# Kernel tuning notes

Hardware: AMD Instinct MI355X
Metric: run time of the kernel (lower is better)

Reference implementation:

```python
import jax, jax.numpy as jnp
import numpy as np

EPS = 1e-12  # tf.math.l2_normalize epsilon

def _l2norm(x):
    # normalize over last axis, matching K.l2_normalize semantics
    sq = jnp.sum(x * x, axis=-1, keepdims=True)
    return x * jax.lax.rsqrt(jnp.maximum(sq, EPS))

def setup_inputs() -> dict:
    key = jax.random.key(0)
    k1, k2, k3 = jax.random.split(key, 3)
    B, L, D, P = 16, 256, 256, 20
    sent1 = jax.random.normal(k1, (B, L, D), dtype=jnp.float32)
    sent2 = jax.random.normal(k2, (B, L, D), dtype=jnp.float32)
    # glorot_uniform for shape (P, D)
    limit = np.sqrt(6.0 / (P + D)).astype(np.float32)
    kernel = jax.random.uniform(k3, (P, D), minval=-limit, maxval=limit, dtype=jnp.float32)
    return {"sent1": sent1, "sent2": sent2, "kernel": kernel}

def reference(sent1, sent2, kernel):
    # sent1: [B,L1,D], sent2: [B,L2,D], kernel: [P,D]
    v1 = _l2norm(sent1[:, :, None, :] * kernel)  # [B,L1,P,D]
    v2 = _l2norm(sent2[:, :, None, :] * kernel)  # [B,L2,P,D]
    # per-perspective cosine similarity matrix: [B,L1,L2,P]
    cos = jnp.einsum('blpd,bmpd->blmp', v1, v2)
    # max over the other sentence's positions (L2) -> [B,L1,P]
    return jnp.max(cos, axis=2)
```

## Files before the change

kernel.cpp:

```cpp
#include <hip/hip_runtime.h>
#include <hip/hip_bf16.h>


#define B_DIM 16
#define L_DIM 256
#define D_DIM 256
#define P_DIM 20
#define TL 64
#define TM 64
#define LDX 264
#define EPS 1e-12f

typedef __attribute__((ext_vector_type(8))) __bf16 bf16x8;
typedef __attribute__((ext_vector_type(4))) float f32x4;

__device__ __forceinline__ unsigned short f2bf(float x) {
  unsigned int u = __float_as_uint(x);
  u += 0x7fffu + ((u >> 16) & 1u);
  return (unsigned short)(u >> 16);
}

__global__ __launch_bounds__(256)
void prep_kernel(const float* __restrict__ s1, const float* __restrict__ s2,
                 const float* __restrict__ kg, float* __restrict__ rn1,
                 float* __restrict__ rn2, unsigned short* __restrict__ s2bf) {
  const int lane = threadIdx.x & 63;
  const int gw   = blockIdx.x * 4 + (threadIdx.x >> 6);
  const int sent = gw >> 12;
  const int row  = gw & 4095;
  const float* src = sent ? s2 : s1;
  float4 sv = *(const float4*)(src + (size_t)row * D_DIM + lane * 4);
  if (sent) {
    unsigned int p0 = ((unsigned int)f2bf(sv.y) << 16) | f2bf(sv.x);
    unsigned int p1 = ((unsigned int)f2bf(sv.w) << 16) | f2bf(sv.z);
    *(uint2*)&s2bf[(size_t)row * D_DIM + lane * 4] = make_uint2(p0, p1);
  }
  float q0 = sv.x * sv.x, q1 = sv.y * sv.y, q2 = sv.z * sv.z, q3 = sv.w * sv.w;
  float* rn = sent ? rn2 : rn1;
  const int b = row >> 8, l = row & 255;
  #pragma unroll 4
  for (int p = 0; p < P_DIM; ++p) {
    float4 kv = *(const float4*)(kg + p * D_DIM + lane * 4);
    float v = q0 * kv.x * kv.x + q1 * kv.y * kv.y + q2 * kv.z * kv.z + q3 * kv.w * kv.w;
    #pragma unroll
    for (int off = 1; off < 64; off <<= 1) v += __shfl_xor(v, off);
    if (lane == 0) rn[((size_t)b * P_DIM + p) * L_DIM + l] = rsqrtf(fmaxf(v, EPS));
  }
}

__global__ __launch_bounds__(256, 2)
void mpm_main(const float* __restrict__ s1, const unsigned short* __restrict__ s2bf,
              const float* __restrict__ kg, const float* __restrict__ rn1,
              const float* __restrict__ rn2, float* __restrict__ outg) {
  __shared__ __align__(16) unsigned short X1[TL * LDX];
  __shared__ __align__(16) unsigned short X2[TM * 256];
  __shared__ float RN1[TL];
  __shared__ float RN2[L_DIM];
  __shared__ float outtmp[2][TL];

  const int tid  = threadIdx.x;
  const int lane = tid & 63;
  const int wave = tid >> 6;
  const int wl = wave & 1, wm = wave >> 1;
  const int lr = lane & 15, q = lane >> 4;

  const int bid = blockIdx.x;
  const int lt = bid & 3;
  const int p  = (bid >> 2) % P_DIM;
  const int b  = bid / (4 * P_DIM);
  const int l0 = lt * TL;

  if (tid < TL) RN1[tid] = rn1[((size_t)b * P_DIM + p) * L_DIM + l0 + tid];
  RN2[tid] = rn2[((size_t)b * P_DIM + p) * L_DIM + tid];
  __syncthreads();

  float4 kv = *(const float4*)(kg + p * D_DIM + lane * 4);
  const float k0 = kv.x * kv.x, k1 = kv.y * kv.y, k2 = kv.z * kv.z, k3 = kv.w * kv.w;

  const float* s1b = s1 + ((size_t)b * L_DIM + l0) * D_DIM;
  #pragma unroll
  for (int i = 0; i < 16; ++i) {
    const int row = i * 4 + wave;
    float4 sv = *(const float4*)(s1b + row * D_DIM + lane * 4);
    float r = RN1[row];
    float x0 = sv.x * k0 * r, x1 = sv.y * k1 * r, x2 = sv.z * k2 * r, x3 = sv.w * k3 * r;
    unsigned int p0 = ((unsigned int)f2bf(x1) << 16) | f2bf(x0);
    unsigned int p1 = ((unsigned int)f2bf(x3) << 16) | f2bf(x2);
    *(uint2*)&X1[row * LDX + lane * 4] = make_uint2(p0, p1);
  }

  float rmax0 = -1e30f, rmax1 = -1e30f;
  const unsigned short* s2b = s2bf + (size_t)b * L_DIM * D_DIM;

  const int baseA0 = (wm * 32 + lr) * 256;
  const int baseA1 = baseA0 + 16 * 256;
  const unsigned short* b0p = &X1[(wl * 32 + lr) * LDX + q * 8];
  const unsigned short* b1p = &X1[(wl * 32 + 16 + lr) * LDX + q * 8];

  for (int mt = 0; mt < L_DIM / TM; ++mt) {
    if (mt) __syncthreads();
    {
      const unsigned short* srcb = s2b + mt * TM * 256;
      unsigned short* ldsb = &X2[wave * 64 * 8];
      #pragma unroll
      for (int j = 0; j < 8; ++j) {
        int sg = j * 256 + tid;
        int r  = sg >> 5, x = sg & 31;
        int c  = x ^ (r & 31);
        const unsigned short* g = srcb + r * 256 + c * 8;
        __builtin_amdgcn_global_load_lds(
            (const __attribute__((address_space(1))) void*)g,
            (__attribute__((address_space(3))) void*)(ldsb + j * 256 * 8),
            16, 0, 0);
      }
    }
    __syncthreads();

    f32x4 acc00 = {0,0,0,0}, acc01 = {0,0,0,0}, acc10 = {0,0,0,0}, acc11 = {0,0,0,0};
    #pragma unroll
    for (int kt = 0; kt < 8; ++kt) {
      const int cc = q + kt * 4;
      bf16x8 a0 = *(const bf16x8*)&X2[baseA0 + ((cc ^ lr) << 3)];
      bf16x8 a1 = *(const bf16x8*)&X2[baseA1 + ((cc ^ lr ^ 16) << 3)];
      bf16x8 b0 = *(const bf16x8*)(b0p + kt * 32);
      bf16x8 b1 = *(const bf16x8*)(b1p + kt * 32);
      acc00 = __builtin_amdgcn_mfma_f32_16x16x32_bf16(a0, b0, acc00, 0, 0, 0);
      acc01 = __builtin_amdgcn_mfma_f32_16x16x32_bf16(a0, b1, acc01, 0, 0, 0);
      acc10 = __builtin_amdgcn_mfma_f32_16x16x32_bf16(a1, b0, acc10, 0, 0, 0);
      acc11 = __builtin_amdgcn_mfma_f32_16x16x32_bf16(a1, b1, acc11, 0, 0, 0);
    }

    #pragma unroll
    for (int r = 0; r < 4; ++r) {
      float rm0 = RN2[mt * TM + wm * 32 + q * 4 + r];
      float rm1 = RN2[mt * TM + wm * 32 + 16 + q * 4 + r];
      rmax0 = fmaxf(rmax0, fmaxf(acc00[r] * rm0, acc10[r] * rm1));
      rmax1 = fmaxf(rmax1, fmaxf(acc01[r] * rm0, acc11[r] * rm1));
    }
  }

  rmax0 = fmaxf(rmax0, __shfl_xor(rmax0, 16));
  rmax0 = fmaxf(rmax0, __shfl_xor(rmax0, 32));
  rmax1 = fmaxf(rmax1, __shfl_xor(rmax1, 16));
  rmax1 = fmaxf(rmax1, __shfl_xor(rmax1, 32));
  if (q == 0) {
    outtmp[wm][wl * 32 + lr]      = rmax0;
    outtmp[wm][wl * 32 + 16 + lr] = rmax1;
  }
  __syncthreads();
  if (tid < TL)
    outg[((size_t)b * L_DIM + (l0 + tid)) * P_DIM + p] =
        fmaxf(outtmp[0][tid], outtmp[1][tid]);
}

extern "C" void kernel_launch(void* const* d_in, const int* in_sizes, int n_in,
                              void* d_out, int out_size, void* d_ws, size_t ws_size,
                              hipStream_t stream) {
  const float* s1 = (const float*)d_in[0];
  const float* s2 = (const float*)d_in[1];
  const float* kg = (const float*)d_in[2];
  float* out = (float*)d_out;

  float* rn1 = (float*)d_ws;
  float* rn2 = rn1 + (size_t)B_DIM * P_DIM * L_DIM;
  unsigned short* s2bf = (unsigned short*)(rn2 + (size_t)B_DIM * P_DIM * L_DIM);

  prep_kernel<<<dim3(2048), dim3(256), 0, stream>>>(s1, s2, kg, rn1, rn2, s2bf);
  mpm_main<<<dim3(B_DIM * P_DIM * (L_DIM / TL)), dim3(256), 0, stream>>>(
      s1, s2bf, kg, rn1, rn2, out);
}
```

Measured before the change: 96.99 us.

## Stage full s2 batch in LDS and loop perspectives per block

Each block now loads the entire bf16 s2 batch into LDS once and keeps its s1 rows in registers, iterating over five perspectives. Each wave computes a 64x64 output tile with 16 accumulators. This removes repeated global/L2 reloads of s2 and s1 across perspectives and m-tiles. In exchange it uses 160KB LDS with one block per CU, has only 256 blocks, and leaves no overlap of the initial load with compute.

```diff
diff --git a/kernel.cpp b/kernel.cpp
--- a/kernel.cpp
+++ b/kernel.cpp
@@ -6,9 +6,6 @@
 #define L_DIM 256
 #define D_DIM 256
 #define P_DIM 20
-#define TL 64
-#define TM 64
-#define LDX 264
 #define EPS 1e-12f
 
 typedef __attribute__((ext_vector_type(8))) __bf16 bf16x8;
@@ -48,109 +45,138 @@
   }
 }
 
-__global__ __launch_bounds__(256, 2)
+__global__ __launch_bounds__(256, 1)
 void mpm_main(const float* __restrict__ s1, const unsigned short* __restrict__ s2bf,
               const float* __restrict__ kg, const float* __restrict__ rn1,
               const float* __restrict__ rn2, float* __restrict__ outg) {
-  __shared__ __align__(16) unsigned short X1[TL * LDX];
-  __shared__ __align__(16) unsigned short X2[TM * 256];
-  __shared__ float RN1[TL];
-  __shared__ float RN2[L_DIM];
-  __shared__ float outtmp[2][TL];
+  __shared__ __align__(16) unsigned short X2[256 * 256];
+  __shared__ __align__(16) unsigned short X1[64 * 256];
+  float* WoutF = (float*)X1;
 
   const int tid  = threadIdx.x;
   const int lane = tid & 63;
   const int wave = tid >> 6;
-  const int wl = wave & 1, wm = wave >> 1;
-  const int lr = lane & 15, q = lane >> 4;
+  const int lr   = lane & 15;
+  const int q    = lane >> 4;
 
   const int bid = blockIdx.x;
-  const int lt = bid & 3;
-  const int p  = (bid >> 2) % P_DIM;
-  const int b  = bid / (4 * P_DIM);
-  const int l0 = lt * TL;
+  const int pgi = bid & 3;
+  const int lt  = (bid >> 2) & 3;
+  const int b   = bid >> 4;
+  const int l0  = lt * 64;
 
-  if (tid < TL) RN1[tid] = rn1[((size_t)b * P_DIM + p) * L_DIM + l0 + tid];
-  RN2[tid] = rn2[((size_t)b * P_DIM + p) * L_DIM + tid];
-  __syncthreads();
-
-  float4 kv = *(const float4*)(kg + p * D_DIM + lane * 4);
-  const float k0 = kv.x * kv.x, k1 = kv.y * kv.y, k2 = kv.z * kv.z, k3 = kv.w * kv.w;
-
-  const float* s1b = s1 + ((size_t)b * L_DIM + l0) * D_DIM;
-  #pragma unroll
-  for (int i = 0; i < 16; ++i) {
-    const int row = i * 4 + wave;
-    float4 sv = *(const float4*)(s1b + row * D_DIM + lane * 4);
-    float r = RN1[row];
-    float x0 = sv.x * k0 * r, x1 = sv.y * k1 * r, x2 = sv.z * k2 * r, x3 = sv.w * k3 * r;
-    unsigned int p0 = ((unsigned int)f2bf(x1) << 16) | f2bf(x0);
-    unsigned int p1 = ((unsigned int)f2bf(x3) << 16) | f2bf(x2);
-    *(uint2*)&X1[row * LDX + lane * 4] = make_uint2(p0, p1);
+  {
+    const unsigned short* s2b = s2bf + (size_t)b * L_DIM * D_DIM;
+    #pragma unroll
+    for (int j = 0; j < 32; ++j) {
+      int g = j * 256 + tid;
+      int r = g >> 5, pr = g & 31;
+      int c = pr ^ (r & 31);
+      __builtin_amdgcn_global_load_lds(
+          (const __attribute__((address_space(1))) void*)(s2b + r * 256 + c * 8),
+          (__attribute__((address_space(3))) void*)(X2 + (size_t)g * 8),
+          16, 0, 0);
+    }
   }
 
-  float rmax0 = -1e30f, rmax1 = -1e30f;
-  const unsigned short* s2b = s2bf + (size_t)b * L_DIM * D_DIM;
+  float4 s1r[16];
+  {
+    const float* s1b = s1 + ((size_t)b * L_DIM + l0) * D_DIM;
+    #pragma unroll
+    for (int i = 0; i < 16; ++i)
+      s1r[i] = *(const float4*)(s1b + (i * 4 + wave) * D_DIM + lane * 4);
+  }
 
-  const int baseA0 = (wm * 32 + lr) * 256;
-  const int baseA1 = baseA0 + 16 * 256;
-  const unsigned short* b0p = &X1[(wl * 32 + lr) * LDX + q * 8];
-  const unsigned short* b1p = &X1[(wl * 32 + 16 + lr) * LDX + q * 8];
+  int mrow[4], mkey[4];
+  #pragma unroll
+  for (int mi = 0; mi < 4; ++mi) {
+    mrow[mi] = wave * 64 + mi * 16 + lr;
+    mkey[mi] = mrow[mi] & 31;
+  }
 
-  for (int mt = 0; mt < L_DIM / TM; ++mt) {
-    if (mt) __syncthreads();
+  #pragma unroll 1
+  for (int pp = 0; pp < 5; ++pp) {
+    const int p = pgi * 5 + pp;
+    __syncthreads();
+
     {
-      const unsigned short* srcb = s2b + mt * TM * 256;
-      unsigned short* ldsb = &X2[wave * 64 * 8];
+      float4 kv = *(const float4*)(kg + p * D_DIM + lane * 4);
+      const float k0 = kv.x * kv.x, k1 = kv.y * kv.y, k2 = kv.z * kv.z, k3 = kv.w * kv.w;
+      const float* rn1b = rn1 + ((size_t)b * P_DIM + p) * L_DIM + l0;
       #pragma unroll
-      for (int j = 0; j < 8; ++j) {
-        int sg = j * 256 + tid;
-        int r  = sg >> 5, x = sg & 31;
-        int c  = x ^ (r & 31);
-        const unsigned short* g = srcb + r * 256 + c * 8;
-        __builtin_amdgcn_global_load_lds(
-            (const __attribute__((address_space(1))) void*)g,
-            (__attribute__((address_space(3))) void*)(ldsb + j * 256 * 8),
-            16, 0, 0);
+      for (int i = 0; i < 16; ++i) {
+        const int row = i * 4 + wave;
+        const float rv = rn1b[row];
+        float x0 = s1r[i].x * k0 * rv, x1 = s1r[i].y * k1 * rv;
+        float x2 = s1r[i].z * k2 * rv, x3 = s1r[i].w * k3 * rv;
+        unsigned int p0 = ((unsigned int)f2bf(x1) << 16) | f2bf(x0);
+        unsigned int p1 = ((unsigned int)f2bf(x3) << 16) | f2bf(x2);
+        *(uint2*)&X1[row * 256 + (((lane >> 1) ^ (row & 31)) << 3) + ((lane & 1) << 2)] =
+            make_uint2(p0, p1);
       }
     }
     __syncthreads();
 
-    f32x4 acc00 = {0,0,0,0}, acc01 = {0,0,0,0}, acc10 = {0,0,0,0}, acc11 = {0,0,0,0};
+    f32x4 acc[4][4];
     #pragma unroll
-    for (int kt = 0; kt < 8; ++kt) {
-      const int cc = q + kt * 4;
-      bf16x8 a0 = *(const bf16x8*)&X2[baseA0 + ((cc ^ lr) << 3)];
-      bf16x8 a1 = *(const bf16x8*)&X2[baseA1 + ((cc ^ lr ^ 16) << 3)];
-      bf16x8 b0 = *(const bf16x8*)(b0p + kt * 32);
-      bf16x8 b1 = *(const bf16x8*)(b1p + kt * 32);
-      acc00 = __builtin_amdgcn_mfma_f32_16x16x32_bf16(a0, b0, acc00, 0, 0, 0);
-      acc01 = __builtin_amdgcn_mfma_f32_16x16x32_bf16(a0, b1, acc01, 0, 0, 0);
-      acc10 = __builtin_amdgcn_mfma_f32_16x16x32_bf16(a1, b0, acc10, 0, 0, 0);
-      acc11 = __builtin_amdgcn_mfma_f32_16x16x32_bf16(a1, b1, acc11, 0, 0, 0);
+    for (int mi = 0; mi < 4; ++mi)
+      #pragma unroll
+      for (int li = 0; li < 4; ++li) acc[mi][li] = (f32x4){0.f, 0.f, 0.f, 0.f};
+
+    #pragma unroll
+    for (int kstep = 0; kstep < 8; ++kstep) {
+      const int cc = kstep * 4 + q;
+      bf16x8 a[4], bb[4];
+      #pragma unroll
+      for (int mi = 0; mi < 4; ++mi)
+        a[mi] = *(const bf16x8*)&X2[mrow[mi] * 256 + ((cc ^ mkey[mi]) << 3)];
+      #pragma unroll
+      for (int li = 0; li < 4; ++li) {
+        const int l = li * 16 + lr;
+        bb[li] = *(const bf16x8*)&X1[l * 256 + ((cc ^ (l & 31)) << 3)];
+      }
+      #pragma unroll
+      for (int mi = 0; mi < 4; ++mi)
+        #pragma unroll
+        for (int li = 0; li < 4; ++li)
+          acc[mi][li] = __builtin_amdgcn_mfma_f32_16x16x32_bf16(a[mi], bb[li], acc[mi][li], 0, 0, 0);
     }
 
+    float4 r2[4];
+    {
+      const float* rn2b = rn2 + ((size_t)b * P_DIM + p) * L_DIM + wave * 64;
+      #pragma unroll
+      for (int mi = 0; mi < 4; ++mi)
+        r2[mi] = *(const float4*)(rn2b + mi * 16 + q * 4);
+    }
+    float v[4];
     #pragma unroll
-    for (int r = 0; r < 4; ++r) {
-      float rm0 = RN2[mt * TM + wm * 32 + q * 4 + r];
-      float rm1 = RN2[mt * TM + wm * 32 + 16 + q * 4 + r];
-      rmax0 = fmaxf(rmax0, fmaxf(acc00[r] * rm0, acc10[r] * rm1));
-      rmax1 = fmaxf(rmax1, fmaxf(acc01[r] * rm0, acc11[r] * rm1));
+    for (int li = 0; li < 4; ++li) {
+      float t = -3.4e38f;
+      #pragma unroll
+      for (int mi = 0; mi < 4; ++mi) {
+        t = fmaxf(t, acc[mi][li][0] * r2[mi].x);
+        t = fmaxf(t, acc[mi][li][1] * r2[mi].y);
+        t = fmaxf(t, acc[mi][li][2] * r2[mi].z);
+        t = fmaxf(t, acc[mi][li][3] * r2[mi].w);
+      }
+      t = fmaxf(t, __shfl_xor(t, 16));
+      t = fmaxf(t, __shfl_xor(t, 32));
+      v[li] = t;
+    }
+
+    __syncthreads();
+    if (q == 0) {
+      #pragma unroll
+      for (int li = 0; li < 4; ++li) WoutF[wave * 64 + li * 16 + lr] = v[li];
+    }
+    __syncthreads();
+    if (tid < 64) {
+      float o = fmaxf(fmaxf(WoutF[tid], WoutF[64 + tid]),
+                      fmaxf(WoutF[128 + tid], WoutF[192 + tid]));
+      outg[((size_t)b * L_DIM + (l0 + tid)) * P_DIM + p] = o;
     }
   }
-
-  rmax0 = fmaxf(rmax0, __shfl_xor(rmax0, 16));
-  rmax0 = fmaxf(rmax0, __shfl_xor(rmax0, 32));
-  rmax1 = fmaxf(rmax1, __shfl_xor(rmax1, 16));
-  rmax1 = fmaxf(rmax1, __shfl_xor(rmax1, 32));
-  if (q == 0) {
-    outtmp[wm][wl * 32 + lr]      = rmax0;
-    outtmp[wm][wl * 32 + 16 + lr] = rmax1;
-  }
-  __syncthreads();
-  if (tid < TL)
-    outg[((size_t)b * L_DIM + (l0 + tid)) * P_DIM + p] =
-        fmaxf(outtmp[0][tid], outtmp[1][tid]);
 }
 
 extern "C" void kernel_launch(void* const* d_in, const int* in_sizes, int n_in,
@@ -166,6 +192,5 @@
   unsigned short* s2bf = (unsigned short*)(rn2 + (size_t)B_DIM * P_DIM * L_DIM);
 
   prep_kernel<<<dim3(2048), dim3(256), 0, stream>>>(s1, s2, kg, rn1, rn2, s2bf);
-  mpm_main<<<dim3(B_DIM * P_DIM * (L_DIM / TL)), dim3(256), 0, stream>>>(
-      s1, s2bf, kg, rn1, rn2, out);
+  mpm_main<<<dim3(256), dim3(256), 0, stream>>>(s1, s2bf, kg, rn1, rn2, out);
 }
```

Result: no change. 96.06 us (-1.0%).
